# Optimization experiments

Measured on AMD Instinct MI355X. Metric: run time of the kernel, lower is better.

## Reference

```python
import jax, jax.numpy as jnp
import numpy as np
from jax import lax

RADIUS = (5, 5, 5)
EPS = 1e-5


def _box_sum(x, radius=RADIUS):
    # Separable all-ones box filter == F.conv3d(x, ones((1,1,)+radius), padding='same')
    # x: [N, 1, D, H, W]
    dn = lax.conv_dimension_numbers(x.shape, (1, 1) + radius, ('NCDHW', 'OIDHW', 'NCDHW'))
    for axis, k in zip((2, 3, 4), radius):
        kshape = [1, 1, 1, 1, 1]
        kshape[axis] = k
        kern = jnp.ones(kshape, dtype=x.dtype)
        dn_ax = lax.conv_dimension_numbers(x.shape, tuple(kshape), ('NCDHW', 'OIDHW', 'NCDHW'))
        x = lax.conv_general_dilated(x, kern, window_strides=(1, 1, 1), padding='SAME',
                                     dimension_numbers=dn_ax)
    return x


def _image_gradient(img):
    # torch.gradient over spatial dims (central diff interior, one-sided edges)
    g = jnp.gradient(img, axis=(2, 3, 4))
    return jnp.concatenate(g, axis=1)  # [N, 3, D, H, W]


def setup_inputs() -> dict:
    key = jax.random.key(0)
    k1, k2, k3, k4 = jax.random.split(key, 4)
    shape = (1, 1, 192, 192, 192)
    moving_image = jax.random.normal(k1, shape, dtype=jnp.float32)
    fixed_image = jax.random.normal(k2, shape, dtype=jnp.float32)
    moving_mask = jax.random.randint(k3, shape, 0, 2).astype(jnp.bool_)
    fixed_mask = jax.random.randint(k4, shape, 0, 2).astype(jnp.bool_)
    original_image_spacing = jnp.ones((3,), dtype=jnp.int32)
    return {
        'moving_image': moving_image,
        'fixed_image': fixed_image,
        'moving_mask': moving_mask,
        'fixed_mask': fixed_mask,
        'original_image_spacing': original_image_spacing,
    }


def reference(moving_image, fixed_image, moving_mask, fixed_mask, original_image_spacing):
    npix = float(np.prod(RADIUS))  # 125

    # dual method: union mask applied to both gradients, total grad halved
    union = jnp.logical_or(moving_mask, fixed_mask).astype(moving_image.dtype)
    grad_moving = _image_gradient(moving_image) * union
    grad_fixed = _image_gradient(fixed_image) * union
    total_grad = (grad_moving + grad_fixed) * 0.5

    sum_m = _box_sum(moving_image)
    sum_f = _box_sum(fixed_image)
    sum_mm = _box_sum(moving_image * moving_image)
    sum_ff = _box_sum(fixed_image * fixed_image)
    sum_mf = _box_sum(moving_image * fixed_image)

    moving_mean = sum_m / npix
    fixed_mean = sum_f / npix

    var_m = sum_mm - 2 * moving_mean * sum_m + npix * moving_mean * moving_mean
    var_f = sum_ff - 2 * fixed_mean * sum_f + npix * fixed_mean * fixed_mean
    var_mf = var_m * var_f
    cross = sum_mf - fixed_mean * sum_m - moving_mean * sum_f + npix * moving_mean * fixed_mean

    moving_mean_centered = moving_image - moving_mean
    fixed_mean_centered = fixed_image - fixed_mean

    mask = (var_mf > EPS) & (var_f > EPS) & (fixed_mean_centered != 0.0) & (moving_mean_centered != 0.0)
    var_mf_safe = jnp.where(mask, var_mf, 1.0)
    var_f_safe = jnp.where(mask, var_f, 1.0)
    factor = jnp.where(
        mask,
        2.0 * cross / var_mf_safe * (moving_mean_centered - cross * fixed_mean_centered / var_f_safe),
        0.0,
    )

    return -1.0 * factor * total_grad
```

## Files before the change

### kernel.cpp

```cpp
#include <hip/hip_runtime.h>


#define DD 192
#define HH 192
#define WW 192
#define NVOX (DD * HH * WW)
#define TS 16
#define RT (TS + 4)
#define ZSEG 24

__global__ __launch_bounds__(256)
void ncc_forces_kernel(const float* __restrict__ mimg,
                       const float* __restrict__ fimg,
                       const int*   __restrict__ mmask,
                       const int*   __restrict__ fmask,
                       float* __restrict__ out)
{
    __shared__ float rawm[4][RT][RT];
    __shared__ float rawf[4][RT][RT];
    __shared__ float xs[5][RT][TS];

    const int tx = threadIdx.x;
    const int ty = threadIdx.y;
    const int tid = ty * TS + tx;
    const int x0 = blockIdx.x * TS;
    const int y0 = blockIdx.y * TS;
    const int z0 = blockIdx.z * ZSEG;
    const int z1 = z0 + ZSEG;

    float ring[5][5];
#pragma unroll
    for (int s = 0; s < 5; ++s)
#pragma unroll
        for (int f = 0; f < 5; ++f) ring[s][f] = 0.f;

    for (int zc = z0 - 2; zc <= z1 + 1; ++zc) {
        const int s4 = (zc + 4) & 3;
        const bool zin = (zc >= 0) && (zc < DD);

        for (int i = tid; i < RT * RT; i += 256) {
            const int iy = i / RT;
            const int ix = i - iy * RT;
            const int gx = x0 - 2 + ix;
            const int gy = y0 - 2 + iy;
            float vm = 0.f, vf = 0.f;
            if (zin && gx >= 0 && gx < WW && gy >= 0 && gy < HH) {
                const int gidx = (zc * HH + gy) * WW + gx;
                vm = mimg[gidx];
                vf = fimg[gidx];
            }
            rawm[s4][iy][ix] = vm;
            rawf[s4][iy][ix] = vf;
        }
        __syncthreads();

        for (int i = tid; i < RT * TS; i += 256) {
            const int y  = i >> 4;
            const int xo = i & 15;
            float sm = 0.f, sf = 0.f, smm = 0.f, sff = 0.f, smf = 0.f;
#pragma unroll
            for (int dx = 0; dx < 5; ++dx) {
                const float a = rawm[s4][y][xo + dx];
                const float b = rawf[s4][y][xo + dx];
                sm += a; sf += b; smm += a * a; sff += b * b; smf += a * b;
            }
            xs[0][y][xo] = sm;
            xs[1][y][xo] = sf;
            xs[2][y][xo] = smm;
            xs[3][y][xo] = sff;
            xs[4][y][xo] = smf;
        }
        __syncthreads();

        float s2d[5];
#pragma unroll
        for (int f = 0; f < 5; ++f) {
            float s = 0.f;
#pragma unroll
            for (int dy = 0; dy < 5; ++dy) s += xs[f][ty + dy][tx];
            s2d[f] = s;
        }
#pragma unroll
        for (int s = 0; s < 4; ++s)
#pragma unroll
            for (int f = 0; f < 5; ++f) ring[s][f] = ring[s + 1][f];
#pragma unroll
        for (int f = 0; f < 5; ++f) ring[4][f] = s2d[f];

        const int z = zc - 2;
        if (z >= z0 && z < z1) {
            float sum_m = 0.f, sum_f = 0.f, sum_mm = 0.f, sum_ff = 0.f, sum_mf = 0.f;
#pragma unroll
            for (int s = 0; s < 5; ++s) {
                sum_m  += ring[s][0];
                sum_f  += ring[s][1];
                sum_mm += ring[s][2];
                sum_ff += ring[s][3];
                sum_mf += ring[s][4];
            }
            const int gx = x0 + tx, gy = y0 + ty;
            const int sz  = (z + 4) & 3;
            const int szm = (z + 3) & 3;
            const int szp = (z + 5) & 3;
            const int cy = ty + 2, cx = tx + 2;
            const float mc = rawm[sz][cy][cx];
            const float fc = rawf[sz][cy][cx];

            float gxm, gxf, gym, gyf, gzm, gzf;
            if (gx == 0)          { gxm = rawm[sz][cy][cx + 1] - mc;  gxf = rawf[sz][cy][cx + 1] - fc; }
            else if (gx == WW-1)  { gxm = mc - rawm[sz][cy][cx - 1];  gxf = fc - rawf[sz][cy][cx - 1]; }
            else {
                gxm = 0.5f * (rawm[sz][cy][cx + 1] - rawm[sz][cy][cx - 1]);
                gxf = 0.5f * (rawf[sz][cy][cx + 1] - rawf[sz][cy][cx - 1]);
            }
            if (gy == 0)          { gym = rawm[sz][cy + 1][cx] - mc;  gyf = rawf[sz][cy + 1][cx] - fc; }
            else if (gy == HH-1)  { gym = mc - rawm[sz][cy - 1][cx];  gyf = fc - rawf[sz][cy - 1][cx]; }
            else {
                gym = 0.5f * (rawm[sz][cy + 1][cx] - rawm[sz][cy - 1][cx]);
                gyf = 0.5f * (rawf[sz][cy + 1][cx] - rawf[sz][cy - 1][cx]);
            }
            if (z == 0)           { gzm = rawm[szp][cy][cx] - mc;     gzf = rawf[szp][cy][cx] - fc; }
            else if (z == DD-1)   { gzm = mc - rawm[szm][cy][cx];     gzf = fc - rawf[szm][cy][cx]; }
            else {
                gzm = 0.5f * (rawm[szp][cy][cx] - rawm[szm][cy][cx]);
                gzf = 0.5f * (rawf[szp][cy][cx] - rawf[szm][cy][cx]);
            }

            const int vidx = (z * HH + gy) * WW + gx;
            const float u = ((mmask[vidx] != 0) || (fmask[vidx] != 0)) ? 1.0f : 0.0f;

            const float npix = 125.0f;
            const float mean_m = sum_m / npix;
            const float mean_f = sum_f / npix;
            const float var_m = sum_mm - 2.0f * mean_m * sum_m + npix * mean_m * mean_m;
            const float var_f = sum_ff - 2.0f * mean_f * sum_f + npix * mean_f * mean_f;
            const float var_mf = var_m * var_f;
            const float cross = sum_mf - mean_f * sum_m - mean_m * sum_f + npix * mean_m * mean_f;
            const float mmc = mc - mean_m;
            const float fmc = fc - mean_f;
            const bool ok = (var_mf > 1e-5f) && (var_f > 1e-5f) && (fmc != 0.0f) && (mmc != 0.0f);
            float factor = 0.0f;
            if (ok) factor = 2.0f * cross / var_mf * (mmc - cross * fmc / var_f);

            const float nf = -factor * 0.5f * u;
            out[vidx]            = nf * (gzm + gzf);
            out[NVOX + vidx]     = nf * (gym + gyf);
            out[2 * NVOX + vidx] = nf * (gxm + gxf);
        }
        __syncthreads();
    }
}

extern "C" void kernel_launch(void* const* d_in, const int* in_sizes, int n_in,
                              void* d_out, int out_size, void* d_ws, size_t ws_size,
                              hipStream_t stream)
{
    const float* mimg  = (const float*)d_in[0];
    const float* fimg  = (const float*)d_in[1];
    const int*   mmask = (const int*)d_in[2];
    const int*   fmask = (const int*)d_in[3];
    float* out = (float*)d_out;

    dim3 grid(WW / TS, HH / TS, DD / ZSEG);
    dim3 block(TS, TS, 1);
    hipLaunchKernelGGL(ncc_forces_kernel, grid, block, 0, stream,
                       mimg, fimg, mmask, fmask, out);
}
```

Before: 258.7 us.

## Prefetch next z-slice via float4 registers and use 5-slot ring to drop barrier

Halo staging now uses 240 threads issuing float4 loads into a padded 24-wide row, and loads slice zc+1 into registers while slice zc is processed. The raw slice ring grows from 4 to 5 slots so the trailing barrier can be removed, and the mask loads are issued early, before the barrier. ZSEG is halved to give more blocks, at the cost of more redundant halo slices per block. The aim is to hide global load latency and cut synchronisation and scalar load instructions.

```diff
diff --git a/kernel.cpp b/kernel.cpp
--- a/kernel.cpp
+++ b/kernel.cpp
@@ -6,8 +6,10 @@
 #define WW 192
 #define NVOX (DD * HH * WW)
 #define TS 16
-#define RT (TS + 4)
-#define ZSEG 24
+#define RR 20
+#define RW 24
+#define ZSEG 12
+#define NRING 5
 
 __global__ __launch_bounds__(256)
 void ncc_forces_kernel(const float* __restrict__ mimg,
@@ -16,9 +18,9 @@
                        const int*   __restrict__ fmask,
                        float* __restrict__ out)
 {
-    __shared__ float rawm[4][RT][RT];
-    __shared__ float rawf[4][RT][RT];
-    __shared__ float xs[5][RT][TS];
+    __shared__ float rawm[NRING][RR][RW];
+    __shared__ float rawf[NRING][RR][RW];
+    __shared__ float xs[5][RR][TS];
 
     const int tx = threadIdx.x;
     const int ty = threadIdx.y;
@@ -28,40 +30,70 @@
     const int z0 = blockIdx.z * ZSEG;
     const int z1 = z0 + ZSEG;
 
+    const int  simg   = tid / 120;
+    const bool stager = (simg < 2);
+    const int  st     = tid - simg * 120;
+    const int  srow   = st / 6;
+    const int  squad  = st - srow * 6;
+    const int  sgy    = y0 - 2 + srow;
+    const int  sgxb   = x0 - 4 + squad * 4;
+    const bool rowin  = (sgy >= 0) && (sgy < HH);
+    const bool fullx  = (sgxb >= 0) && (sgxb + 3 < WW);
+    const float* simg_ptr = (simg == 1) ? fimg : mimg;
+    float* slds_base = (simg == 1) ? &rawf[0][0][0] : &rawm[0][0][0];
+    const int  sloff = srow * RW + squad * 4;
+
+    auto prefetch = [&](int zc_, float4& p) {
+        p.x = p.y = p.z = p.w = 0.f;
+        if (stager && rowin && zc_ >= 0 && zc_ < DD) {
+            const float* src = simg_ptr + ((size_t)zc_ * HH + sgy) * WW;
+            if (fullx) {
+                p = *(const float4*)(src + sgxb);
+            } else {
+                if (sgxb + 0 >= 0 && sgxb + 0 < WW) p.x = src[sgxb + 0];
+                if (sgxb + 1 >= 0 && sgxb + 1 < WW) p.y = src[sgxb + 1];
+                if (sgxb + 2 >= 0 && sgxb + 2 < WW) p.z = src[sgxb + 2];
+                if (sgxb + 3 >= 0 && sgxb + 3 < WW) p.w = src[sgxb + 3];
+            }
+        }
+    };
+
     float ring[5][5];
 #pragma unroll
     for (int s = 0; s < 5; ++s)
 #pragma unroll
         for (int f = 0; f < 5; ++f) ring[s][f] = 0.f;
 
+    float4 pref;
+    prefetch(z0 - 2, pref);
+
     for (int zc = z0 - 2; zc <= z1 + 1; ++zc) {
-        const int s4 = (zc + 4) & 3;
-        const bool zin = (zc >= 0) && (zc < DD);
-
-        for (int i = tid; i < RT * RT; i += 256) {
-            const int iy = i / RT;
-            const int ix = i - iy * RT;
-            const int gx = x0 - 2 + ix;
-            const int gy = y0 - 2 + iy;
-            float vm = 0.f, vf = 0.f;
-            if (zin && gx >= 0 && gx < WW && gy >= 0 && gy < HH) {
-                const int gidx = (zc * HH + gy) * WW + gx;
-                vm = mimg[gidx];
-                vf = fimg[gidx];
-            }
-            rawm[s4][iy][ix] = vm;
-            rawf[s4][iy][ix] = vf;
-        }
+        const int sw = (zc + 10) % 5;
+
+        if (stager) {
+            *(float4*)(slds_base + sw * (RR * RW) + sloff) = pref;
+        }
+        prefetch(zc + 1, pref);
+
+        const int z = zc - 2;
+        const bool emitv = (z >= z0) && (z < z1);
+        int um = 0, uf = 0;
+        if (emitv) {
+            const int vidx = (z * HH + (y0 + ty)) * WW + (x0 + tx);
+            um = mmask[vidx];
+            uf = fmask[vidx];
+        }
+
         __syncthreads();
 
-        for (int i = tid; i < RT * TS; i += 256) {
+        for (int i = tid; i < RR * TS; i += 256) {
             const int y  = i >> 4;
             const int xo = i & 15;
             float sm = 0.f, sf = 0.f, smm = 0.f, sff = 0.f, smf = 0.f;
 #pragma unroll
             for (int dx = 0; dx < 5; ++dx) {
-                const float a = rawm[s4][y][xo + dx];
-                const float b = rawf[s4][y][xo + dx];
+                const float a = rawm[sw][y][xo + 2 + dx];
+                const float b = rawf[sw][y][xo + 2 + dx];
                 sm += a; sf += b; smm += a * a; sff += b * b; smf += a * b;
             }
             xs[0][y][xo] = sm;
@@ -70,6 +102,7 @@
             xs[3][y][xo] = sff;
             xs[4][y][xo] = smf;
         }
+
         __syncthreads();
 
         float s2d[5];
@@ -87,8 +120,7 @@
 #pragma unroll
         for (int f = 0; f < 5; ++f) ring[4][f] = s2d[f];
 
-        const int z = zc - 2;
-        if (z >= z0 && z < z1) {
+        if (emitv) {
             float sum_m = 0.f, sum_f = 0.f, sum_mm = 0.f, sum_ff = 0.f, sum_mf = 0.f;
 #pragma unroll
             for (int s = 0; s < 5; ++s) {
@@ -99,10 +131,10 @@
                 sum_mf += ring[s][4];
             }
             const int gx = x0 + tx, gy = y0 + ty;
-            const int sz  = (z + 4) & 3;
-            const int szm = (z + 3) & 3;
-            const int szp = (z + 5) & 3;
-            const int cy = ty + 2, cx = tx + 2;
+            const int sz  = (zc + 8) % 5;
+            const int szm = (zc + 7) % 5;
+            const int szp = (zc + 9) % 5;
+            const int cy = ty + 2, cx = tx + 4;
             const float mc = rawm[sz][cy][cx];
             const float fc = rawf[sz][cy][cx];
 
@@ -126,12 +158,12 @@
                 gzf = 0.5f * (rawf[szp][cy][cx] - rawf[szm][cy][cx]);
             }
 
-            const int vidx = (z * HH + gy) * WW + gx;
-            const float u = ((mmask[vidx] != 0) || (fmask[vidx] != 0)) ? 1.0f : 0.0f;
+            const float u = ((um != 0) || (uf != 0)) ? 1.0f : 0.0f;
 
             const float npix = 125.0f;
-            const float mean_m = sum_m / npix;
-            const float mean_f = sum_f / npix;
+            const float inv_npix = 1.0f / 125.0f;
+            const float mean_m = sum_m * inv_npix;
+            const float mean_f = sum_f * inv_npix;
             const float var_m = sum_mm - 2.0f * mean_m * sum_m + npix * mean_m * mean_m;
             const float var_f = sum_ff - 2.0f * mean_f * sum_f + npix * mean_f * mean_f;
             const float var_mf = var_m * var_f;
@@ -142,12 +174,12 @@
             float factor = 0.0f;
             if (ok) factor = 2.0f * cross / var_mf * (mmc - cross * fmc / var_f);
 
+            const int vidx = (z * HH + gy) * WW + gx;
             const float nf = -factor * 0.5f * u;
             out[vidx]            = nf * (gzm + gzf);
             out[NVOX + vidx]     = nf * (gym + gyf);
             out[2 * NVOX + vidx] = nf * (gxm + gxf);
         }
-        __syncthreads();
     }
 }
 
```

Measured after the change: 230.0 us. -11.1%, faster.
